# Kernel tuning notes

Hardware: AMD Instinct MI355X
Metric: run time of the kernel (lower is better)

## Reference

```python
import jax, jax.numpy as jnp
import numpy as np

N_NODES = 50000
IN_FEAT = 64
HIDDEN = 128
SCALAR_DIM = 64
VECTOR_DIM = 32
N_EDGES = 800000
INPUT_DIM = 3 * IN_FEAT + 1  # 193


def _mlp(x, W1, b1, W2, b2):
    # Linear -> ReLU -> Linear (make_mlp)
    h = jax.nn.relu(x @ W1 + b1)
    return h @ W2 + b2


def setup_inputs() -> dict:
    key = jax.random.key(0)
    ks = jax.random.split(key, 12)
    s = lambda fan_in: 1.0 / np.sqrt(fan_in)
    return {
        "endpoints": jax.random.randint(ks[0], (N_EDGES, 2), 0, N_NODES, dtype=jnp.int64),
        "edge_lengths": jax.random.uniform(ks[1], (N_EDGES, 1), dtype=jnp.float32),
        "midpoint_theta": jax.random.normal(ks[2], (N_EDGES,), dtype=jnp.float32),
        "endpoint_features": jax.random.normal(ks[3], (N_NODES, IN_FEAT), dtype=jnp.float32),
        "W1s": jax.random.normal(ks[4], (INPUT_DIM, HIDDEN), dtype=jnp.float32) * s(INPUT_DIM),
        "b1s": jnp.zeros((HIDDEN,), dtype=jnp.float32),
        "W2s": jax.random.normal(ks[5], (HIDDEN, SCALAR_DIM), dtype=jnp.float32) * s(HIDDEN),
        "b2s": jnp.zeros((SCALAR_DIM,), dtype=jnp.float32),
        "W1v": jax.random.normal(ks[6], (INPUT_DIM, HIDDEN), dtype=jnp.float32) * s(INPUT_DIM),
        "b1v": jnp.zeros((HIDDEN,), dtype=jnp.float32),
        "W2v": jax.random.normal(ks[7], (HIDDEN, VECTOR_DIM), dtype=jnp.float32) * s(HIDDEN),
        "b2v": jnp.zeros((VECTOR_DIM,), dtype=jnp.float32),
    }


def reference(endpoints, edge_lengths, midpoint_theta, endpoint_features,
              W1s, b1s, W2s, b2s, W1v, b1v, W2v, b2v):
    i = endpoints[:, 0]
    j = endpoints[:, 1]
    feat_i = endpoint_features[i]            # [E, F] gather
    feat_j = endpoint_features[j]            # [E, F] gather
    diff = jnp.abs(feat_i - feat_j)          # [E, F]
    inputs = jnp.concatenate([feat_i, feat_j, diff, edge_lengths], axis=-1)  # [E, 3F+1]
    h0 = _mlp(inputs, W1s, b1s, W2s, b2s)    # [E, scalar_dim]
    direction = jnp.stack([jnp.cos(midpoint_theta), jnp.sin(midpoint_theta)], axis=-1)  # [E, 2]
    amplitude = _mlp(inputs, W1v, b1v, W2v, b2v)[..., None]  # [E, vector_dim, 1]
    v0 = amplitude * direction[:, None, :]   # [E, vector_dim, 2]
    return (h0, v0)
```

## Files before the change

### kernel.cpp

```cpp
#include <hip/hip_runtime.h>
#include <hip/hip_bf16.h>

#define N_EDGES 800000
#define M_BLK   64
#define NBLK    (N_EDGES / M_BLK)
#define XS      200
#define HS      136

typedef __attribute__((ext_vector_type(8))) _Float16 half8;
typedef __attribute__((ext_vector_type(4))) float    f32x4;

__global__ void prep_kernel(const float* __restrict__ W1s, const float* __restrict__ W1v,
                            const float* __restrict__ W2s, const float* __restrict__ W2v,
                            _Float16* __restrict__ wt1s, _Float16* __restrict__ wt1v,
                            _Float16* __restrict__ wt2s, _Float16* __restrict__ wt2v,
                            float* __restrict__ w1s192, float* __restrict__ w1v192)
{
    int idx = blockIdx.x * blockDim.x + threadIdx.x;
    if (idx < 128 * 192) {
        int c = idx / 192, k = idx % 192;
        wt1s[idx] = (_Float16)W1s[k * 128 + c];
        wt1v[idx] = (_Float16)W1v[k * 128 + c];
        return;
    }
    int i2 = idx - 128 * 192;
    if (i2 >= 0 && i2 < 64 * 128) {
        int c = i2 / 128, k = i2 % 128;
        wt2s[i2] = (_Float16)W2s[k * 64 + c];
        return;
    }
    int i3 = idx - (128 * 192 + 64 * 128);
    if (i3 >= 0 && i3 < 32 * 128) {
        int c = i3 / 128, k = i3 % 128;
        wt2v[i3] = (_Float16)W2v[k * 32 + c];
        return;
    }
    int i4 = idx - (128 * 192 + 64 * 128 + 32 * 128);
    if (i4 >= 0 && i4 < 128) {
        w1s192[i4] = W1s[192 * 128 + i4];
        w1v192[i4] = W1v[192 * 128 + i4];
    }
}

__global__ __launch_bounds__(512) void edge_mlp_kernel(
    const int*   __restrict__ endpoints,
    const float* __restrict__ edge_len,
    const float* __restrict__ theta,
    const float* __restrict__ feat,
    const float* __restrict__ b1s, const float* __restrict__ b2s,
    const float* __restrict__ b1v, const float* __restrict__ b2v,
    const _Float16* __restrict__ wt1s, const _Float16* __restrict__ wt1v,
    const _Float16* __restrict__ wt2s, const _Float16* __restrict__ wt2v,
    const float* __restrict__ w1s192, const float* __restrict__ w1v192,
    float* __restrict__ h0, float* __restrict__ v0)
{
    __shared__ _Float16 ldsX[M_BLK * XS];
    __shared__ _Float16 ldsHs[M_BLK * HS];
    __shared__ float    ldsLen[M_BLK];
    __shared__ float2   ldsDir[M_BLK];

    const int t   = threadIdx.x;
    const int blk = blockIdx.x;
    const int w   = t >> 6;
    const int l   = t & 63;
    const int lr  = l & 15;
    const int lk  = l >> 4;

    const int c1 = w * 16 + lr;
    half8 bs[6], bv[6];
#pragma unroll
    for (int ks = 0; ks < 6; ++ks) {
        bs[ks] = *reinterpret_cast<const half8*>(wt1s + c1 * 192 + ks * 32 + lk * 8);
        bv[ks] = *reinterpret_cast<const half8*>(wt1v + c1 * 192 + ks * 32 + lk * 8);
    }

    {
        const int e  = t >> 3;
        const int f0 = (t & 7) * 8;
        const int ge = blk * M_BLK + e;
        const int vi = endpoints[2 * ge];
        const int vj = endpoints[2 * ge + 1];
        const float4* fi = reinterpret_cast<const float4*>(feat + (size_t)vi * 64 + f0);
        const float4* fj = reinterpret_cast<const float4*>(feat + (size_t)vj * 64 + f0);
        float4 a0 = fi[0], a1 = fi[1];
        float4 b0 = fj[0], b1 = fj[1];
        float ai[8] = {a0.x, a0.y, a0.z, a0.w, a1.x, a1.y, a1.z, a1.w};
        float bj[8] = {b0.x, b0.y, b0.z, b0.w, b1.x, b1.y, b1.z, b1.w};
        half8 pi, pj, pd;
#pragma unroll
        for (int q = 0; q < 8; ++q) {
            pi[q] = (_Float16)ai[q];
            pj[q] = (_Float16)bj[q];
            pd[q] = (_Float16)fabsf(ai[q] - bj[q]);
        }
        *reinterpret_cast<half8*>(&ldsX[e * XS + f0])       = pi;
        *reinterpret_cast<half8*>(&ldsX[e * XS + 64 + f0])  = pj;
        *reinterpret_cast<half8*>(&ldsX[e * XS + 128 + f0]) = pd;

        if (t < M_BLK) {
            ldsLen[t] = edge_len[blk * M_BLK + t];
        } else if (t < 2 * M_BLK) {
            int ee = t - M_BLK;
            float th = theta[blk * M_BLK + ee];
            ldsDir[ee] = make_float2(cosf(th), sinf(th));
        }
    }
    __syncthreads();

    f32x4 accs[4], accv[4];
#pragma unroll
    for (int rt = 0; rt < 4; ++rt) {
        accs[rt] = (f32x4){0.f, 0.f, 0.f, 0.f};
        accv[rt] = (f32x4){0.f, 0.f, 0.f, 0.f};
    }
#pragma unroll
    for (int rt = 0; rt < 4; ++rt) {
#pragma unroll
        for (int ks = 0; ks < 6; ++ks) {
            half8 a = *reinterpret_cast<const half8*>(&ldsX[(rt * 16 + lr) * XS + ks * 32 + lk * 8]);
            accs[rt] = __builtin_amdgcn_mfma_f32_16x16x32_f16(a, bs[ks], accs[rt], 0, 0, 0);
            accv[rt] = __builtin_amdgcn_mfma_f32_16x16x32_f16(a, bv[ks], accv[rt], 0, 0, 0);
        }
    }

    const float b1s_c   = b1s[c1];
    const float b1v_c   = b1v[c1];
    const float w192s_c = w1s192[c1];
    const float w192v_c = w1v192[c1];
    __syncthreads();
    _Float16* ldsHv = ldsX;
#pragma unroll
    for (int rt = 0; rt < 4; ++rt) {
#pragma unroll
        for (int r = 0; r < 4; ++r) {
            int row = rt * 16 + lk * 4 + r;
            float len = ldsLen[row];
            float hs = accs[rt][r] + b1s_c + len * w192s_c;
            float hv = accv[rt][r] + b1v_c + len * w192v_c;
            ldsHs[row * HS + c1] = (_Float16)fmaxf(hs, 0.f);
            ldsHv[row * HS + c1] = (_Float16)fmaxf(hv, 0.f);
        }
    }
    __syncthreads();

    const int rt2 = w >> 1;
    const int ch  = w & 1;

    half8 a2[4];
#pragma unroll
    for (int ks = 0; ks < 4; ++ks)
        a2[ks] = *reinterpret_cast<const half8*>(&ldsHs[(rt2 * 16 + lr) * HS + ks * 32 + lk * 8]);
    f32x4 acc2[2];
    acc2[0] = (f32x4){0.f, 0.f, 0.f, 0.f};
    acc2[1] = (f32x4){0.f, 0.f, 0.f, 0.f};
#pragma unroll
    for (int ct = 0; ct < 2; ++ct) {
        int c2 = ch * 32 + ct * 16 + lr;
#pragma unroll
        for (int ks = 0; ks < 4; ++ks) {
            half8 b = *reinterpret_cast<const half8*>(wt2s + c2 * 128 + ks * 32 + lk * 8);
            acc2[ct] = __builtin_amdgcn_mfma_f32_16x16x32_f16(a2[ks], b, acc2[ct], 0, 0, 0);
        }
    }
#pragma unroll
    for (int ct = 0; ct < 2; ++ct) {
        int c2 = ch * 32 + ct * 16 + lr;
        float bias = b2s[c2];
#pragma unroll
        for (int r = 0; r < 4; ++r) {
            int row = rt2 * 16 + lk * 4 + r;
            h0[(size_t)(blk * M_BLK + row) * 64 + c2] = acc2[ct][r] + bias;
        }
    }

    f32x4 accV = (f32x4){0.f, 0.f, 0.f, 0.f};
    const int cv = ch * 16 + lr;
#pragma unroll
    for (int ks = 0; ks < 4; ++ks) {
        half8 a = *reinterpret_cast<const half8*>(&ldsHv[(rt2 * 16 + lr) * HS + ks * 32 + lk * 8]);
        half8 b = *reinterpret_cast<const half8*>(wt2v + cv * 128 + ks * 32 + lk * 8);
        accV = __builtin_amdgcn_mfma_f32_16x16x32_f16(a, b, accV, 0, 0, 0);
    }
    const float biasv = b2v[cv];
#pragma unroll
    for (int r = 0; r < 4; ++r) {
        int row = rt2 * 16 + lk * 4 + r;
        float amp = accV[r] + biasv;
        float2 d = ldsDir[row];
        *reinterpret_cast<float2*>(v0 + ((size_t)(blk * M_BLK + row) * 32 + cv) * 2) =
            make_float2(amp * d.x, amp * d.y);
    }
}

extern "C" void kernel_launch(void* const* d_in, const int* in_sizes, int n_in,
                              void* d_out, int out_size, void* d_ws, size_t ws_size,
                              hipStream_t stream)
{
    const int*   endpoints = (const int*)d_in[0];
    const float* edge_len  = (const float*)d_in[1];
    const float* theta     = (const float*)d_in[2];
    const float* feat      = (const float*)d_in[3];
    const float* W1s       = (const float*)d_in[4];
    const float* b1s       = (const float*)d_in[5];
    const float* W2s       = (const float*)d_in[6];
    const float* b2s       = (const float*)d_in[7];
    const float* W1v       = (const float*)d_in[8];
    const float* b1v       = (const float*)d_in[9];
    const float* W2v       = (const float*)d_in[10];
    const float* b2v       = (const float*)d_in[11];

    char* ws = (char*)d_ws;
    _Float16* wt1s   = (_Float16*)(ws);
    _Float16* wt1v   = (_Float16*)(ws + 49152);
    _Float16* wt2s   = (_Float16*)(ws + 98304);
    _Float16* wt2v   = (_Float16*)(ws + 114688);
    float*    w1s192 = (float*)(ws + 122880);
    float*    w1v192 = (float*)(ws + 123392);

    prep_kernel<<<145, 256, 0, stream>>>(W1s, W1v, W2s, W2v,
                                         wt1s, wt1v, wt2s, wt2v, w1s192, w1v192);

    float* h0 = (float*)d_out;
    float* v0 = h0 + (size_t)N_EDGES * 64;
    edge_mlp_kernel<<<NBLK, 512, 0, stream>>>(endpoints, edge_len, theta, feat,
                                              b1s, b2s, b1v, b2v,
                                              wt1s, wt1v, wt2s, wt2v,
                                              w1s192, w1v192, h0, v0);
}
```

Baseline: 338.2 us.

## Process four edge tiles per block with prefetched gathers and swizzled LDS

Each block now loops over four 64-edge tiles instead of one, prefetching the next tile's feature gathers and endpoint indices while the current tile's MFMA work runs. LDS rows are XOR-swizzled instead of padded to avoid bank conflicts, the LDS footprint is reduced by aliasing X/Hs, and launch bounds request higher occupancy. Layer-1 weights are reloaded from global/L2 per ks step instead of held in registers, trading register pressure for extra loads, and the block count drops fourfold, which may reduce parallelism.

New measurement: 861.3 us. 2.55x slower.

```diff
diff --git a/kernel.cpp b/kernel.cpp
--- a/kernel.cpp
+++ b/kernel.cpp
@@ -3,9 +3,9 @@
 
 #define N_EDGES 800000
 #define M_BLK   64
-#define NBLK    (N_EDGES / M_BLK)
-#define XS      200
-#define HS      136
+#define TILES   4
+#define EPB     (M_BLK * TILES)
+#define NBLK    (N_EDGES / EPB)
 
 typedef __attribute__((ext_vector_type(8))) _Float16 half8;
 typedef __attribute__((ext_vector_type(4))) float    f32x4;
@@ -42,7 +42,14 @@
     }
 }
 
-__global__ __launch_bounds__(512) void edge_mlp_kernel(
+__device__ __forceinline__ void* xsw(char* base, int row, int byte_in_row, int row_bytes)
+{
+    int chunk = byte_in_row >> 4;
+    int sw    = ((chunk ^ (row & 7)) << 4) | (byte_in_row & 15);
+    return (void*)(base + row * row_bytes + sw);
+}
+
+__global__ __launch_bounds__(512, 6) void edge_mlp_kernel(
     const int*   __restrict__ endpoints,
     const float* __restrict__ edge_len,
     const float* __restrict__ theta,
@@ -54,10 +61,12 @@
     const float* __restrict__ w1s192, const float* __restrict__ w1v192,
     float* __restrict__ h0, float* __restrict__ v0)
 {
-    __shared__ _Float16 ldsX[M_BLK * XS];
-    __shared__ _Float16 ldsHs[M_BLK * HS];
-    __shared__ float    ldsLen[M_BLK];
-    __shared__ float2   ldsDir[M_BLK];
+    __shared__ char lds[33536];
+    char* X  = lds;
+    char* Hs = lds;
+    char* Hv = lds + 16384;
+    float*  Len = (float*)(lds + 32768);
+    float2* Dir = (float2*)(lds + 33024);
 
     const int t   = threadIdx.x;
     const int blk = blockIdx.x;
@@ -65,130 +74,142 @@
     const int l   = t & 63;
     const int lr  = l & 15;
     const int lk  = l >> 4;
+    const int e   = t >> 3;
+    const int f0q = t & 7;
+    const int base = blk * EPB;
 
     const int c1 = w * 16 + lr;
-    half8 bs[6], bv[6];
-#pragma unroll
-    for (int ks = 0; ks < 6; ++ks) {
-        bs[ks] = *reinterpret_cast<const half8*>(wt1s + c1 * 192 + ks * 32 + lk * 8);
-        bv[ks] = *reinterpret_cast<const half8*>(wt1v + c1 * 192 + ks * 32 + lk * 8);
-    }
-
-    {
-        const int e  = t >> 3;
-        const int f0 = (t & 7) * 8;
-        const int ge = blk * M_BLK + e;
-        const int vi = endpoints[2 * ge];
-        const int vj = endpoints[2 * ge + 1];
-        const float4* fi = reinterpret_cast<const float4*>(feat + (size_t)vi * 64 + f0);
-        const float4* fj = reinterpret_cast<const float4*>(feat + (size_t)vj * 64 + f0);
-        float4 a0 = fi[0], a1 = fi[1];
-        float4 b0 = fj[0], b1 = fj[1];
-        float ai[8] = {a0.x, a0.y, a0.z, a0.w, a1.x, a1.y, a1.z, a1.w};
-        float bj[8] = {b0.x, b0.y, b0.z, b0.w, b1.x, b1.y, b1.z, b1.w};
-        half8 pi, pj, pd;
-#pragma unroll
-        for (int q = 0; q < 8; ++q) {
-            pi[q] = (_Float16)ai[q];
-            pj[q] = (_Float16)bj[q];
-            pd[q] = (_Float16)fabsf(ai[q] - bj[q]);
-        }
-        *reinterpret_cast<half8*>(&ldsX[e * XS + f0])       = pi;
-        *reinterpret_cast<half8*>(&ldsX[e * XS + 64 + f0])  = pj;
-        *reinterpret_cast<half8*>(&ldsX[e * XS + 128 + f0]) = pd;
-
-        if (t < M_BLK) {
-            ldsLen[t] = edge_len[blk * M_BLK + t];
-        } else if (t < 2 * M_BLK) {
-            int ee = t - M_BLK;
-            float th = theta[blk * M_BLK + ee];
-            ldsDir[ee] = make_float2(cosf(th), sinf(th));
-        }
-    }
-    __syncthreads();
-
-    f32x4 accs[4], accv[4];
-#pragma unroll
-    for (int rt = 0; rt < 4; ++rt) {
-        accs[rt] = (f32x4){0.f, 0.f, 0.f, 0.f};
-        accv[rt] = (f32x4){0.f, 0.f, 0.f, 0.f};
-    }
-#pragma unroll
-    for (int rt = 0; rt < 4; ++rt) {
-#pragma unroll
-        for (int ks = 0; ks < 6; ++ks) {
-            half8 a = *reinterpret_cast<const half8*>(&ldsX[(rt * 16 + lr) * XS + ks * 32 + lk * 8]);
-            accs[rt] = __builtin_amdgcn_mfma_f32_16x16x32_f16(a, bs[ks], accs[rt], 0, 0, 0);
-            accv[rt] = __builtin_amdgcn_mfma_f32_16x16x32_f16(a, bv[ks], accv[rt], 0, 0, 0);
-        }
-    }
-
     const float b1s_c   = b1s[c1];
     const float b1v_c   = b1v[c1];
     const float w192s_c = w1s192[c1];
     const float w192v_c = w1v192[c1];
-    __syncthreads();
-    _Float16* ldsHv = ldsX;
-#pragma unroll
-    for (int rt = 0; rt < 4; ++rt) {
-#pragma unroll
-        for (int r = 0; r < 4; ++r) {
-            int row = rt * 16 + lk * 4 + r;
-            float len = ldsLen[row];
-            float hs = accs[rt][r] + b1s_c + len * w192s_c;
-            float hv = accv[rt][r] + b1v_c + len * w192v_c;
-            ldsHs[row * HS + c1] = (_Float16)fmaxf(hs, 0.f);
-            ldsHv[row * HS + c1] = (_Float16)fmaxf(hv, 0.f);
-        }
-    }
-    __syncthreads();
 
     const int rt2 = w >> 1;
     const int ch  = w & 1;
-
-    half8 a2[4];
-#pragma unroll
-    for (int ks = 0; ks < 4; ++ks)
-        a2[ks] = *reinterpret_cast<const half8*>(&ldsHs[(rt2 * 16 + lr) * HS + ks * 32 + lk * 8]);
-    f32x4 acc2[2];
-    acc2[0] = (f32x4){0.f, 0.f, 0.f, 0.f};
-    acc2[1] = (f32x4){0.f, 0.f, 0.f, 0.f};
-#pragma unroll
-    for (int ct = 0; ct < 2; ++ct) {
-        int c2 = ch * 32 + ct * 16 + lr;
-#pragma unroll
-        for (int ks = 0; ks < 4; ++ks) {
-            half8 b = *reinterpret_cast<const half8*>(wt2s + c2 * 128 + ks * 32 + lk * 8);
-            acc2[ct] = __builtin_amdgcn_mfma_f32_16x16x32_f16(a2[ks], b, acc2[ct], 0, 0, 0);
-        }
-    }
-#pragma unroll
-    for (int ct = 0; ct < 2; ++ct) {
-        int c2 = ch * 32 + ct * 16 + lr;
-        float bias = b2s[c2];
-#pragma unroll
-        for (int r = 0; r < 4; ++r) {
-            int row = rt2 * 16 + lk * 4 + r;
-            h0[(size_t)(blk * M_BLK + row) * 64 + c2] = acc2[ct][r] + bias;
-        }
-    }
-
-    f32x4 accV = (f32x4){0.f, 0.f, 0.f, 0.f};
-    const int cv = ch * 16 + lr;
-#pragma unroll
-    for (int ks = 0; ks < 4; ++ks) {
-        half8 a = *reinterpret_cast<const half8*>(&ldsHv[(rt2 * 16 + lr) * HS + ks * 32 + lk * 8]);
-        half8 b = *reinterpret_cast<const half8*>(wt2v + cv * 128 + ks * 32 + lk * 8);
-        accV = __builtin_amdgcn_mfma_f32_16x16x32_f16(a, b, accV, 0, 0, 0);
-    }
-    const float biasv = b2v[cv];
-#pragma unroll
-    for (int r = 0; r < 4; ++r) {
-        int row = rt2 * 16 + lk * 4 + r;
-        float amp = accV[r] + biasv;
-        float2 d = ldsDir[row];
-        *reinterpret_cast<float2*>(v0 + ((size_t)(blk * M_BLK + row) * 32 + cv) * 2) =
-            make_float2(amp * d.x, amp * d.y);
+    const float b2s_a = b2s[ch * 32 + lr];
+    const float b2s_b = b2s[ch * 32 + 16 + lr];
+    const float b2v_c = b2v[ch * 16 + lr];
+
+    float4 fi0, fi1, fj0, fj1;
+    float  len_pf = 0.f, th_pf = 0.f;
+    {
+        int2 ep0 = ((const int2*)endpoints)[base + e];
+        const float* pfi = feat + (size_t)ep0.x * 64 + f0q * 8;
+        const float* pfj = feat + (size_t)ep0.y * 64 + f0q * 8;
+        fi0 = ((const float4*)pfi)[0]; fi1 = ((const float4*)pfi)[1];
+        fj0 = ((const float4*)pfj)[0]; fj1 = ((const float4*)pfj)[1];
+        if (t < M_BLK)          len_pf = edge_len[base + t];
+        else if (t < 2 * M_BLK) th_pf  = theta[base + (t - M_BLK)];
+    }
+    int2 epA = ((const int2*)endpoints)[base + 1 * M_BLK + e];
+    int2 epB = ((const int2*)endpoints)[base + 2 * M_BLK + e];
+
+    for (int tile = 0; tile < TILES; ++tile) {
+        {
+            float ai[8] = {fi0.x, fi0.y, fi0.z, fi0.w, fi1.x, fi1.y, fi1.z, fi1.w};
+            float bj[8] = {fj0.x, fj0.y, fj0.z, fj0.w, fj1.x, fj1.y, fj1.z, fj1.w};
+            half8 pi, pj, pd;
+#pragma unroll
+            for (int q = 0; q < 8; ++q) {
+                pi[q] = (_Float16)ai[q];
+                pj[q] = (_Float16)bj[q];
+                pd[q] = (_Float16)fabsf(ai[q] - bj[q]);
+            }
+            *(half8*)xsw(X, e, f0q * 16, 384)       = pi;
+            *(half8*)xsw(X, e, 128 + f0q * 16, 384) = pj;
+            *(half8*)xsw(X, e, 256 + f0q * 16, 384) = pd;
+            if (t < M_BLK)          Len[t] = len_pf;
+            else if (t < 2 * M_BLK) Dir[t - M_BLK] = make_float2(cosf(th_pf), sinf(th_pf));
+        }
+        __syncthreads();
+
+        if (tile + 1 < TILES) {
+            const float* pfi = feat + (size_t)epA.x * 64 + f0q * 8;
+            const float* pfj = feat + (size_t)epA.y * 64 + f0q * 8;
+            fi0 = ((const float4*)pfi)[0]; fi1 = ((const float4*)pfi)[1];
+            fj0 = ((const float4*)pfj)[0]; fj1 = ((const float4*)pfj)[1];
+            if (t < M_BLK)          len_pf = edge_len[base + (tile + 1) * M_BLK + t];
+            else if (t < 2 * M_BLK) th_pf  = theta[base + (tile + 1) * M_BLK + (t - M_BLK)];
+        }
+        epA = epB;
+        if (tile + 3 < TILES)
+            epB = ((const int2*)endpoints)[base + (tile + 3) * M_BLK + e];
+
+        f32x4 accs[4], accv[4];
+#pragma unroll
+        for (int rt = 0; rt < 4; ++rt) {
+            accs[rt] = (f32x4){0.f, 0.f, 0.f, 0.f};
+            accv[rt] = (f32x4){0.f, 0.f, 0.f, 0.f};
+        }
+        const _Float16* pws = wt1s + c1 * 192 + lk * 8;
+        const _Float16* pwv = wt1v + c1 * 192 + lk * 8;
+#pragma unroll
+        for (int ks = 0; ks < 6; ++ks) {
+            half8 bs = *reinterpret_cast<const half8*>(pws + ks * 32);
+            half8 bv = *reinterpret_cast<const half8*>(pwv + ks * 32);
+#pragma unroll
+            for (int rt = 0; rt < 4; ++rt) {
+                half8 a = *(half8*)xsw(X, rt * 16 + lr, ks * 64 + lk * 16, 384);
+                accs[rt] = __builtin_amdgcn_mfma_f32_16x16x32_f16(a, bs, accs[rt], 0, 0, 0);
+                accv[rt] = __builtin_amdgcn_mfma_f32_16x16x32_f16(a, bv, accv[rt], 0, 0, 0);
+            }
+        }
+        __syncthreads();
+
+#pragma unroll
+        for (int rt = 0; rt < 4; ++rt) {
+#pragma unroll
+            for (int r = 0; r < 4; ++r) {
+                int row = rt * 16 + lk * 4 + r;
+                float len = Len[row];
+                float hs = accs[rt][r] + b1s_c + len * w192s_c;
+                float hv = accv[rt][r] + b1v_c + len * w192v_c;
+                *(_Float16*)xsw(Hs, row, c1 * 2, 256) = (_Float16)fmaxf(hs, 0.f);
+                *(_Float16*)xsw(Hv, row, c1 * 2, 256) = (_Float16)fmaxf(hv, 0.f);
+            }
+        }
+        __syncthreads();
+
+        {
+            f32x4 acc2[2];
+            acc2[0] = (f32x4){0.f, 0.f, 0.f, 0.f};
+            acc2[1] = (f32x4){0.f, 0.f, 0.f, 0.f};
+            f32x4 accV = (f32x4){0.f, 0.f, 0.f, 0.f};
+            const int cv = ch * 16 + lr;
+#pragma unroll
+            for (int ks = 0; ks < 4; ++ks) {
+                half8 a2 = *(half8*)xsw(Hs, rt2 * 16 + lr, ks * 64 + lk * 16, 256);
+#pragma unroll
+                for (int ct = 0; ct < 2; ++ct) {
+                    int c2 = ch * 32 + ct * 16 + lr;
+                    half8 b = *reinterpret_cast<const half8*>(wt2s + c2 * 128 + ks * 32 + lk * 8);
+                    acc2[ct] = __builtin_amdgcn_mfma_f32_16x16x32_f16(a2, b, acc2[ct], 0, 0, 0);
+                }
+                half8 av = *(half8*)xsw(Hv, rt2 * 16 + lr, ks * 64 + lk * 16, 256);
+                half8 bv2 = *reinterpret_cast<const half8*>(wt2v + cv * 128 + ks * 32 + lk * 8);
+                accV = __builtin_amdgcn_mfma_f32_16x16x32_f16(av, bv2, accV, 0, 0, 0);
+            }
+            const size_t grow0 = (size_t)(base + tile * M_BLK);
+#pragma unroll
+            for (int ct = 0; ct < 2; ++ct) {
+                int c2 = ch * 32 + ct * 16 + lr;
+                float bias = ct ? b2s_b : b2s_a;
+#pragma unroll
+                for (int r = 0; r < 4; ++r) {
+                    int row = rt2 * 16 + lk * 4 + r;
+                    h0[(grow0 + row) * 64 + c2] = acc2[ct][r] + bias;
+                }
+            }
+#pragma unroll
+            for (int r = 0; r < 4; ++r) {
+                int row = rt2 * 16 + lk * 4 + r;
+                float amp = accV[r] + b2v_c;
+                float2 d = Dir[row];
+                *reinterpret_cast<float2*>(v0 + ((grow0 + row) * 32 + cv) * 2) =
+                    make_float2(amp * d.x, amp * d.y);
+            }
+        }
+        __syncthreads();
     }
 }
 
```
